# Performance work log

Measured on AMD Instinct MI355X. Metric: run time of the kernel, lower is better.

## Reference

```python
import jax, jax.numpy as jnp
import numpy as np

B, C, H, W = 4, 512, 96, 96
NH = 8
HD = C // NH
NC = 128
D = 768
L = H * W
EPS = 1e-5  # torch LayerNorm default


def _l2n(x, axis):
    # F.normalize: x / max(||x||, 1e-12)
    return x / jnp.maximum(jnp.linalg.norm(x, axis=axis, keepdims=True), 1e-12)


def _ln2d(x, g, b):
    # LayerNorm2d: normalize over channel dim of (B,C,H,W)
    mu = x.mean(1, keepdims=True)
    var = ((x - mu) ** 2).mean(1, keepdims=True)
    return (x - mu) / jnp.sqrt(var + EPS) * g[None, :, None, None] + b[None, :, None, None]


def _conv1x1(x, w):
    return jnp.einsum('oc,bchw->bohw', w, x)


def setup_inputs() -> dict:
    key = jax.random.key(0)
    ks = jax.random.split(key, 9)
    s = 0.02
    return {
        'img_feats': jax.random.normal(ks[0], (B, C, H, W), jnp.float32),
        'cls_embs': jax.random.normal(ks[1], (NC, D), jnp.float32),
        'cls_logits': jax.random.normal(ks[2], (B, NC), jnp.float32),
        'seg_logits': jax.random.normal(ks[3], (B, 1, H, W), jnp.float32),
        'gamma_g': jnp.ones((D,), jnp.float32), 'beta_g': jnp.zeros((D,), jnp.float32),
        'gamma_f': jnp.ones((C,), jnp.float32), 'beta_f': jnp.zeros((C,), jnp.float32),
        'attn_scale': jnp.ones((NH, 1, 1), jnp.float32),
        'Wg': jax.random.normal(ks[4], (C, D), jnp.float32) * s,
        'Wqkv': jax.random.normal(ks[5], (3 * C, C), jnp.float32) * s,
        'Wo': jax.random.normal(ks[6], (C, C), jnp.float32) * s,
        'bo': jnp.zeros((C,), jnp.float32),
        'gamma_n': jnp.ones((C,), jnp.float32), 'beta_n': jnp.zeros((C,), jnp.float32),
        'W1': jax.random.normal(ks[7], (C, C), jnp.float32) * s, 'b1': jnp.zeros((C,), jnp.float32),
        'W2': jax.random.normal(ks[8], (C, C), jnp.float32) * s, 'b2': jnp.zeros((C,), jnp.float32),
    }


def reference(img_feats, cls_embs, cls_logits, seg_logits, gamma_g, beta_g,
              gamma_f, beta_f, attn_scale, Wg, Wqkv, Wo, bo, gamma_n, beta_n,
              W1, b1, W2, b2):
    xn = _ln2d(img_feats, gamma_f, beta_f)
    # guide LayerNorm over embedding dim
    mu = cls_embs.mean(-1, keepdims=True)
    var = ((cls_embs - mu) ** 2).mean(-1, keepdims=True)
    cn = (cls_embs - mu) / jnp.sqrt(var + EPS) * gamma_g + beta_g
    g = (cn @ Wg.T).reshape(NC, NH, HD)  # nc nh hd

    qkv = _conv1x1(xn, Wqkv).reshape(B, 3, NH, HD, L)
    q, k, v = qkv[:, 0], qkv[:, 1], qkv[:, 2]  # each (B,NH,HD,L)

    # cosine guide map + min-max normalization + softmax-weighted aggregation over classes
    gm = jnp.einsum('nhd,bhdl->bhnl', _l2n(g, -1), _l2n(q, -2))
    gm = gm - gm.min(-1, keepdims=True)
    gm = gm / gm.max(-1, keepdims=True)
    gm = (jax.nn.softmax(gm, axis=2) * gm).sum(2, keepdims=True)  # (B,NH,1,L)

    # auxiliary guide map from cls logits + masked pooling of k
    cls_obj = jnp.einsum('nhd,bn->bhd', g, cls_logits)
    mask = jax.nn.sigmoid(seg_logits)  # (B,1,H,W)
    seg_obj = (mask * k.reshape(B, C, H, W)).sum((2, 3)) / mask.sum((2, 3))  # (B,C)
    obj = _l2n(cls_obj + seg_obj.reshape(B, NH, HD), -1)
    aux = jnp.einsum('bhd,bhdl->bhl', obj, _l2n(k, -2))[:, :, None, :]
    aux = aux - aux.min(-1, keepdims=True)
    aux = aux / aux.max(-1, keepdims=True)
    gm = gm * aux

    v = gm * v
    # channel (transposed) cosine attention: (B,NH,HD,HD)
    attn = jnp.einsum('bhdl,bhel->bhde', _l2n(q, -1), _l2n(k, -1)) * attn_scale
    out = jnp.einsum('bhde,bhel->bhdl', jax.nn.softmax(attn, -1), v).reshape(B, C, H, W)

    x = img_feats + _conv1x1(out, Wo) + bo[None, :, None, None]
    # ConvMlp with pre-norm: LayerNorm2d -> 1x1 conv -> GELU -> 1x1 conv
    fin = _ln2d(x, gamma_n, beta_n)
    h = jax.nn.gelu(_conv1x1(fin, W1) + b1[None, :, None, None], approximate=False)
    return x + _conv1x1(h, W2) + b2[None, :, None, None]
```

## Files before the change

kernel.cpp:

```cpp
#include <hip/hip_runtime.h>
#include <hip/hip_bf16.h>
#include <math.h>

#define BB 4
#define CC 512
#define NHEAD 8
#define HDIM 64
#define NCLS 128
#define DD 768
#define LL 9216
#define BLPIX 36864
#define EPSV 1e-5f
#define GMBLK 144
#define AUXBLK 144
#define LSPLIT 8
#define NLT 72
#define TP 132

typedef __hip_bfloat16 bf16;
typedef __attribute__((ext_vector_type(8))) short short8v;
typedef __attribute__((ext_vector_type(4))) short short4v;
typedef __attribute__((ext_vector_type(4))) float f32x4;

__device__ __forceinline__ float bf2f(bf16 v){ return __bfloat162float(v); }
__device__ __forceinline__ bf16 f2bf(float v){ return __float2bfloat16(v); }
__device__ __forceinline__ short bfbits(float v){ bf16 b = __float2bfloat16(v); return *reinterpret_cast<short*>(&b); }
__device__ __forceinline__ float s2f(short s){ bf16 b = *reinterpret_cast<bf16*>(&s); return __bfloat162float(b); }

__global__ __launch_bounds__(256) void wclsg_k(
    const float* __restrict__ wqkv, const float* __restrict__ wo,
    const float* __restrict__ w1, const float* __restrict__ w2,
    bf16* __restrict__ oq, bf16* __restrict__ oo,
    bf16* __restrict__ o1, bf16* __restrict__ o2,
    const float* __restrict__ cls_embs, const float* __restrict__ gamma_g,
    const float* __restrict__ beta_g, const float* __restrict__ Wg,
    float* __restrict__ g, bf16* __restrict__ gnb)
{
  __shared__ __align__(16) float cn[DD];
  __shared__ float red[256];
  __shared__ float gsh[CC];
  __shared__ float nrm[NHEAD];
  int bid = blockIdx.x;
  int tid = threadIdx.x;
  if (bid < 1536){
    int i = bid * 256 + tid;
    int e = i * 4;
    const float* src; bf16* dst; int off;
    if (e < 786432){ src = wqkv; dst = oq; off = e; }
    else if (e < 1048576){ src = wo; dst = oo; off = e - 786432; }
    else if (e < 1310720){ src = w1; dst = o1; off = e - 1048576; }
    else { src = w2; dst = o2; off = e - 1310720; }
    float4 v = *reinterpret_cast<const float4*>(src + off);
    short4v pk;
    pk[0] = bfbits(v.x); pk[1] = bfbits(v.y); pk[2] = bfbits(v.z); pk[3] = bfbits(v.w);
    *(short4v*)&dst[off] = pk;
    return;
  }
  {
    int n = bid - 1536;
    const float* e = cls_embs + (size_t)n * DD;
    float s = 0.f, ss = 0.f;
    for (int i = tid; i < DD; i += 256){ float v = e[i]; s += v; ss += v * v; }
    red[tid] = s; __syncthreads();
    for (int st = 128; st > 0; st >>= 1){ if (tid < st) red[tid] += red[tid + st]; __syncthreads(); }
    float mean = red[0] / DD; __syncthreads();
    red[tid] = ss; __syncthreads();
    for (int st = 128; st > 0; st >>= 1){ if (tid < st) red[tid] += red[tid + st]; __syncthreads(); }
    float var = red[0] / DD - mean * mean;
    float rstd = rsqrtf(var + EPSV);
    __syncthreads();
    for (int i = tid; i < DD; i += 256) cn[i] = (e[i] - mean) * rstd * gamma_g[i] + beta_g[i];
    __syncthreads();
    for (int c = tid; c < CC; c += 256){
      const float* w = Wg + (size_t)c * DD;
      float a = 0.f;
      #pragma unroll 8
      for (int d = 0; d < DD; d++) a += cn[d] * w[d];
      gsh[c] = a;
    }
    __syncthreads();
    if (tid < NHEAD){
      float a = 0.f;
      for (int d = 0; d < HDIM; d++){ float v = gsh[tid * HDIM + d]; a += v * v; }
      nrm[tid] = fmaxf(sqrtf(a), 1e-12f);
    }
    __syncthreads();
    for (int c = tid; c < CC; c += 256){
      g[(size_t)n * CC + c] = gsh[c];
      gnb[(size_t)n * CC + c] = f2bf(gsh[c] / nrm[c >> 6]);
    }
  }
}

__global__ __launch_bounds__(256, 2) void fuse_ln_k(const float* __restrict__ X,
    const float* __restrict__ lng, const float* __restrict__ lnb,
    bf16* __restrict__ xnT){
  __shared__ bf16 st[512][68];
  __shared__ float sred[2][4][64];
  __shared__ float muS[64], rsS[64];
  int p0 = blockIdx.x * 64;
  int b = p0 / LL, l0 = p0 - b * LL;
  int tid = threadIdx.x;
  #pragma unroll 4
  for (int i = 0; i < 32; i++){
    int idx = i * 256 + tid;
    int c = idx >> 4, l4 = (idx & 15) * 4;
    float4 v = *reinterpret_cast<const float4*>(X + (size_t)b * CC * LL + (size_t)c * LL + l0 + l4);
    short4v pk;
    pk[0] = bfbits(v.x); pk[1] = bfbits(v.y); pk[2] = bfbits(v.z); pk[3] = bfbits(v.w);
    *(short4v*)&st[c][l4] = pk;
  }
  __syncthreads();
  {
    int cg = tid >> 6, l = tid & 63;
    float s = 0.f, ss = 0.f;
    for (int c = cg * 128; c < cg * 128 + 128; c++){
      float v = bf2f(st[c][l]);
      s += v; ss += v * v;
    }
    sred[0][cg][l] = s; sred[1][cg][l] = ss;
  }
  __syncthreads();
  if (tid < 64){
    float st2 = sred[0][0][tid] + sred[0][1][tid] + sred[0][2][tid] + sred[0][3][tid];
    float sst = sred[1][0][tid] + sred[1][1][tid] + sred[1][2][tid] + sred[1][3][tid];
    float m = st2 * (1.0f / CC);
    float var = sst * (1.0f / CC) - m * m;
    muS[tid] = m; rsS[tid] = rsqrtf(var + EPSV);
  }
  __syncthreads();
  int pr = tid >> 4;
  int cc = (tid & 15) * 4;
  for (int cb = 0; cb < 8; cb++){
    int c0 = cb * 64;
    #pragma unroll
    for (int i = 0; i < 4; i++){
      int pl = pr + i * 16;
      int p = p0 + pl;
      float m = muS[pl], r = rsS[pl];
      short4v pk;
      #pragma unroll
      for (int e = 0; e < 4; e++){
        int c = c0 + cc + e;
        pk[e] = bfbits((bf2f(st[c][pl]) - m) * r * lng[c] + lnb[c]);
      }
      *(short4v*)&xnT[(size_t)p * CC + c0 + cc] = pk;
    }
  }
}

template<int MODE>
__global__ __launch_bounds__(256, 2) void mgemm_k(
    const bf16* __restrict__ A,
    const bf16* __restrict__ B,
    const float* __restrict__ residf,
    const bf16* __restrict__ residb,
    const float* __restrict__ bias,
    const float* __restrict__ lng, const float* __restrict__ lnb,
    float2* __restrict__ statp,
    float* __restrict__ qssp, float* __restrict__ kssp,
    bf16* __restrict__ qTo, float* __restrict__ rqo,
    bf16* __restrict__ ko, bf16* __restrict__ vo,
    bf16* __restrict__ xT_out,
    float* __restrict__ xo,
    bf16* __restrict__ ho,
    const float* __restrict__ gA, const float* __restrict__ clsl, float* __restrict__ clsovO,
    const float* __restrict__ segf, float* __restrict__ segpO)
{
  __shared__ __align__(16) short smem[128 * TP];
  __shared__ float sredf[512];
  short* Asm = smem;
  short* Bsm = smem + 8192;
  short* T   = smem;
  int tid = threadIdx.x;
  if (MODE == 0 && blockIdx.x >= 3456){
    int idx = (blockIdx.x - 3456) * 256 + tid;
    int b = idx >> 9, c = idx & 511;
    float a = 0.f;
    for (int n = 0; n < NCLS; n++) a += gA[(size_t)n * CC + c] * clsl[b * NCLS + n];
    clsovO[idx] = a;
    return;
  }
  int lane = tid & 63, wv = tid >> 6;
  int wr = wv >> 1, wc = wv & 1;
  int r15 = lane & 15, g = lane >> 4, h7 = lane & 7;
  int flat, gx, cpx;
  if (MODE == 0){ flat = blockIdx.x; gx = 12; cpx = 432; }
  else { gx = gridDim.x; flat = blockIdx.y * gx + blockIdx.x; cpx = (gx * gridDim.y) >> 3; }
  int swz = (flat & 7) * cpx + (flat >> 3);
  int m0 = (swz % gx) * 128, n0 = (swz / gx) * 128;
  int srow = tid >> 3, skkg = tid & 7;
  int sslot = ((skkg ^ (srow & 7))) * 8;

  f32x4 acc[4][4];
  #pragma unroll
  for (int i = 0; i < 4; i++)
    #pragma unroll
    for (int j = 0; j < 4; j++) acc[i][j] = (f32x4){0.f, 0.f, 0.f, 0.f};

  if (MODE == 2){
    if (tid < 128){
      int p = n0 + tid;
      float s = 0.f, ss2 = 0.f;
      #pragma unroll
      for (int part = 0; part < 4; part++){
        float2 v = statp[part * BLPIX + p];
        s += v.x; ss2 += v.y;
      }
      float m = s * (1.0f / CC);
      float var = ss2 * (1.0f / CC) - m * m;
      sredf[tid] = m;
      sredf[128 + tid] = rsqrtf(var + EPSV);
    }
    __syncthreads();
  }

  short8v pa[4], pb[4];
  auto loadAB = [&](int it){
    int k0 = it * 64;
    if (MODE == 2){
      int c0 = k0 + skkg * 8;
      float ga[8], be[8];
      *(float4*)&ga[0] = *(const float4*)&lng[c0];
      *(float4*)&ga[4] = *(const float4*)&lng[c0 + 4];
      *(float4*)&be[0] = *(const float4*)&lnb[c0];
      *(float4*)&be[4] = *(const float4*)&lnb[c0 + 4];
      #pragma unroll
      for (int r = 0; r < 4; r++){
        pa[r] = *reinterpret_cast<const short8v*>(A + (size_t)(m0 + r * 32 + srow) * 512 + c0);
        int rl = r * 32 + srow;
        float mm = sredf[rl], rr = sredf[128 + rl];
        short8v rawv = *reinterpret_cast<const short8v*>(B + (size_t)(n0 + rl) * 512 + c0);
        short8v ov;
        #pragma unroll
        for (int e = 0; e < 8; e++){
          float v = (s2f(rawv[e]) - mm) * rr * ga[e] + be[e];
          ov[e] = bfbits(v);
        }
        pb[r] = ov;
      }
    } else {
      #pragma unroll
      for (int r = 0; r < 4; r++){
        pa[r] = *reinterpret_cast<const short8v*>(A + (size_t)(m0 + r * 32 + srow) * 512 + k0 + skkg * 8);
        pb[r] = *reinterpret_cast<const short8v*>(B + (size_t)(n0 + r * 32 + srow) * 512 + k0 + skkg * 8);
      }
    }
  };

  loadAB(0);
  for (int it = 0; it < 8; ++it){
    __syncthreads();
    #pragma unroll
    for (int r = 0; r < 4; r++){
      int row = r * 32 + srow;
      *(short8v*)&Asm[row * 64 + sslot] = pa[r];
      *(short8v*)&Bsm[row * 64 + sslot] = pb[r];
    }
    __syncthreads();
    if (it < 7) loadAB(it + 1);
    #pragma unroll
    for (int s = 0; s < 2; s++){
      int slot = ((s * 4 + g) ^ h7) * 8;
      short8v af[4], bf_[4];
      #pragma unroll
      for (int i = 0; i < 4; i++){
        af[i]  = *(const short8v*)&Asm[(wr * 64 + i * 16 + r15) * 64 + slot];
        bf_[i] = *(const short8v*)&Bsm[(wc * 64 + i * 16 + r15) * 64 + slot];
      }
      #pragma unroll
      for (int i = 0; i < 4; i++)
        #pragma unroll
        for (int j = 0; j < 4; j++){
          if (MODE == 2)
            acc[i][j] = __builtin_amdgcn_mfma_f32_16x16x32_bf16(bf_[i], af[j], acc[i][j], 0, 0, 0);
          else
            acc[i][j] = __builtin_amdgcn_mfma_f32_16x16x32_bf16(af[i], bf_[j], acc[i][j], 0, 0, 0);
        }
    }
  }

  int bIdx = n0 / LL;
  int lbase = n0 - bIdx * LL;
  if (MODE == 0){
    int part = m0 >> 9;
    if (part == 0){
      int chb = m0 + wr * 64;
      int head = chb >> 6;
      int bh = bIdx * 8 + head;
      #pragma unroll
      for (int j = 0; j < 4; j++){
        float ssl = 0.f;
        #pragma unroll
        for (int i = 0; i < 4; i++)
          #pragma unroll
          for (int e = 0; e < 4; e++) ssl += acc[i][j][e] * acc[i][j][e];
        ssl += __shfl_xor(ssl, 16); ssl += __shfl_xor(ssl, 32);
        if (g == 0){
          int l = lbase + wc * 64 + j * 16 + r15;
          rqo[(size_t)bh * LL + l] = 1.0f / fmaxf(sqrtf(ssl), 1e-12f);
        }
      }
      #pragma unroll
      for (int i = 0; i < 4; i++)
        #pragma unroll
        for (int e = 0; e < 4; e++){
          float ssv = acc[i][0][e]*acc[i][0][e] + acc[i][1][e]*acc[i][1][e]
                    + acc[i][2][e]*acc[i][2][e] + acc[i][3][e]*acc[i][3][e];
          #pragma unroll
          for (int msk = 1; msk < 16; msk <<= 1) ssv += __shfl_xor(ssv, msk);
          if (r15 == 0) sredf[wv * 64 + i * 16 + g * 4 + e] = ssv;
        }
      __syncthreads();
      if (tid < 128){
        int wrr = tid >> 6, chL = tid & 63;
        float tot = sredf[(wrr * 2) * 64 + chL] + sredf[(wrr * 2 + 1) * 64 + chL];
        int c = m0 + wrr * 64 + chL;
        int row = bIdx * 512 + c;
        int ltile = lbase >> 7;
        qssp[(size_t)row * NLT + ltile] = tot;
      }
      #pragma unroll
      for (int i = 0; i < 4; i++)
        #pragma unroll
        for (int j = 0; j < 4; j++){
          int pxl = wc * 64 + j * 16 + r15;
          int chl = wr * 64 + i * 16 + g * 4;
          short4v pk;
          #pragma unroll
          for (int e = 0; e < 4; e++) pk[e] = bfbits(acc[i][j][e]);
          *(short4v*)&T[pxl * TP + chl] = pk;
        }
      __syncthreads();
      #pragma unroll
      for (int it2 = 0; it2 < 16; it2++){
        int c2 = tid + it2 * 256;
        int px = c2 >> 5, ch4 = (c2 & 31) * 4;
        *(short4v*)&qTo[((size_t)bIdx * LL + lbase + px) * CC + m0 + ch4] = *(short4v*)&T[px * TP + ch4];
      }
    } else if (part == 1){
      int chb = (m0 & 511) + wr * 64;
      #pragma unroll
      for (int i = 0; i < 4; i++)
        #pragma unroll
        for (int j = 0; j < 4; j++){
          int l = lbase + wc * 64 + j * 16 + r15;
          #pragma unroll
          for (int e = 0; e < 4; e++){
            int ch = chb + i * 16 + g * 4 + e;
            ko[(size_t)bIdx * CC * LL + (size_t)ch * LL + l] = f2bf(acc[i][j][e]);
          }
        }
      float sg[4];
      #pragma unroll
      for (int j = 0; j < 4; j++){
        int l = lbase + wc * 64 + j * 16 + r15;
        sg[j] = 1.0f / (1.0f + expf(-segf[(size_t)bIdx * LL + l]));
      }
      #pragma unroll
      for (int i = 0; i < 4; i++)
        #pragma unroll
        for (int e = 0; e < 4; e++){
          float ssv = acc[i][0][e]*acc[i][0][e] + acc[i][1][e]*acc[i][1][e]
                    + acc[i][2][e]*acc[i][2][e] + acc[i][3][e]*acc[i][3][e];
          float sgv = sg[0]*acc[i][0][e] + sg[1]*acc[i][1][e]
                    + sg[2]*acc[i][2][e] + sg[3]*acc[i][3][e];
          #pragma unroll
          for (int msk = 1; msk < 16; msk <<= 1){
            ssv += __shfl_xor(ssv, msk);
            sgv += __shfl_xor(sgv, msk);
          }
          if (r15 == 0){
            sredf[wv * 64 + i * 16 + g * 4 + e] = ssv;
            sredf[256 + wv * 64 + i * 16 + g * 4 + e] = sgv;
          }
        }
      __syncthreads();
      if (tid < 128){
        int wrr = tid >> 6, chL = tid & 63;
        float tot  = sredf[(wrr * 2) * 64 + chL] + sredf[(wrr * 2 + 1) * 64 + chL];
        float tots = sredf[256 + (wrr * 2) * 64 + chL] + sredf[256 + (wrr * 2 + 1) * 64 + chL];
        int c = (m0 & 511) + wrr * 64 + chL;
        int row = bIdx * 512 + c;
        int ltile = lbase >> 7;
        kssp[(size_t)row * NLT + ltile] = tot;
        segpO[(size_t)row * NLT + ltile] = tots;
      }
    } else {
      __syncthreads();
      #pragma unroll
      for (int i = 0; i < 4; i++)
        #pragma unroll
        for (int j = 0; j < 4; j++){
          int pxl = wc * 64 + j * 16 + r15;
          int chl = wr * 64 + i * 16 + g * 4;
          short4v pk;
          #pragma unroll
          for (int e = 0; e < 4; e++) pk[e] = bfbits(acc[i][j][e]);
          *(short4v*)&T[pxl * TP + chl] = pk;
        }
      __syncthreads();
      int chg = (m0 & 511);
      #pragma unroll
      for (int it2 = 0; it2 < 16; it2++){
        int c2 = tid + it2 * 256;
        int px = c2 >> 5, ch4 = (c2 & 31) * 4;
        *(short4v*)&vo[((size_t)bIdx * LL + lbase + px) * CC + chg + ch4] = *(short4v*)&T[px * TP + ch4];
      }
    }
  } else if (MODE == 1){
    __syncthreads();
    float sj[4] = {0.f,0.f,0.f,0.f}, ssj[4] = {0.f,0.f,0.f,0.f};
    #pragma unroll
    for (int i = 0; i < 4; i++)
      #pragma unroll
      for (int j = 0; j < 4; j++){
        int l = lbase + wc * 64 + j * 16 + r15;
        int chm = m0 + wr * 64 + i * 16 + g * 4;
        int pxl = wc * 64 + j * 16 + r15;
        int chl = wr * 64 + i * 16 + g * 4;
        short4v pk;
        #pragma unroll
        for (int e = 0; e < 4; e++){
          int m = chm + e;
          size_t o = (size_t)bIdx * CC * LL + (size_t)m * LL + l;
          float xv = residf[o] + acc[i][j][e] + bias[m];
          pk[e] = bfbits(xv);
          sj[j] += xv; ssj[j] += xv * xv;
        }
        *(short4v*)&T[pxl * TP + chl] = pk;
      }
    #pragma unroll
    for (int j = 0; j < 4; j++){
      sj[j] += __shfl_xor(sj[j], 16); sj[j] += __shfl_xor(sj[j], 32);
      ssj[j] += __shfl_xor(ssj[j], 16); ssj[j] += __shfl_xor(ssj[j], 32);
    }
    if (g == 0){
      #pragma unroll
      for (int j = 0; j < 4; j++){
        sredf[wv * 128 + j * 32 + r15 * 2 + 0] = sj[j];
        sredf[wv * 128 + j * 32 + r15 * 2 + 1] = ssj[j];
      }
    }
    __syncthreads();
    if (tid < 128){
      int wv2 = tid >> 6, lane2 = tid & 63, j2 = lane2 >> 4, r2 = lane2 & 15;
      float s   = sredf[wv2 * 128 + j2 * 32 + r2 * 2 + 0] + sredf[(wv2 + 2) * 128 + j2 * 32 + r2 * 2 + 0];
      float ss2 = sredf[wv2 * 128 + j2 * 32 + r2 * 2 + 1] + sredf[(wv2 + 2) * 128 + j2 * 32 + r2 * 2 + 1];
      int p = n0 + wv2 * 64 + j2 * 16 + r2;
      statp[(m0 >> 7) * BLPIX + p] = make_float2(s, ss2);
    }
    #pragma unroll
    for (int it2 = 0; it2 < 16; it2++){
      int c2 = tid + it2 * 256;
      int px = c2 >> 5, ch4 = (c2 & 31) * 4;
      *(short4v*)&xT_out[((size_t)bIdx * LL + lbase + px) * CC + m0 + ch4] = *(short4v*)&T[px * TP + ch4];
    }
  } else if (MODE == 3){
    __syncthreads();
    #pragma unroll
    for (int it2 = 0; it2 < 16; it2++){
      int c2 = tid + it2 * 256;
      int px = c2 >> 5, ch4 = (c2 & 31) * 4;
      *(short4v*)&T[px * TP + ch4] = *(const short4v*)&residb[((size_t)bIdx * LL + lbase + px) * CC + m0 + ch4];
    }
    __syncthreads();
    #pragma unroll
    for (int i = 0; i < 4; i++)
      #pragma unroll
      for (int j = 0; j < 4; j++){
        int l = lbase + wc * 64 + j * 16 + r15;
        int chm = m0 + wr * 64 + i * 16 + g * 4;
        int pxl = wc * 64 + j * 16 + r15;
        int chl = wr * 64 + i * 16 + g * 4;
        short4v rv = *(short4v*)&T[pxl * TP + chl];
        #pragma unroll
        for (int e = 0; e < 4; e++){
          int m = chm + e;
          size_t o = (size_t)bIdx * CC * LL + (size_t)m * LL + l;
          xo[o] = s2f(rv[e]) + acc[i][j][e] + bias[m];
        }
      }
  } else {
    #pragma unroll
    for (int i = 0; i < 4; i++)
      #pragma unroll
      for (int j = 0; j < 4; j++){
        int mm = m0 + wr * 64 + j * 16 + r15;
        float bv = bias[mm];
        #pragma unroll
        for (int e = 0; e < 4; e++){
          int n = n0 + wc * 64 + i * 16 + g * 4 + e;
          float t = acc[i][j][e] + bv;
          float gv = 0.5f * t * (1.0f + erff(t * 0.70710678118654752f));
          ho[(size_t)n * CC + mm] = f2bf(gv);
        }
      }
  }
}

__global__ __launch_bounds__(256) void mega1_k(
    const bf16* __restrict__ qT, const float* __restrict__ rq,
    const bf16* __restrict__ k, const bf16* __restrict__ gnb,
    float* __restrict__ pmin, float* __restrict__ pmax,
    float* __restrict__ part,
    const float* __restrict__ seg, float* __restrict__ seg_num, float* __restrict__ den,
    const float* __restrict__ qssp, const float* __restrict__ kssp,
    const float* __restrict__ segp,
    float* __restrict__ qn, float* __restrict__ kn)
{
  __shared__ __align__(16) bf16 qs[128 * 68];
  int bid = blockIdx.x;
  int t = threadIdx.x;
  if (bid < 1152){
    int bh = bid & 31, ltg = bid >> 5;
    int b = bh >> 3, h = bh & 7;
    int w = t >> 6, lane = t & 63, r15 = lane & 15, g = lane >> 4;
    short8v ag[2][2];
    #pragma unroll
    for (int i = 0; i < 2; i++)
      #pragma unroll
      for (int kt = 0; kt < 2; kt++)
        ag[i][kt] = *reinterpret_cast<const short8v*>(gnb + (size_t)(w * 32 + i * 16 + r15) * CC + h * 64 + kt * 32 + g * 8);
    for (int sub = 0; sub < 4; sub++){
      int lt = ltg * 4 + sub;
      int l0 = lt * 64;
      const bf16* qTp = qT + ((size_t)(b * LL + l0)) * CC + h * 64;
      short8v bq[4][2];
      float rqv[4];
      #pragma unroll
      for (int j = 0; j < 4; j++){
        #pragma unroll
        for (int kt = 0; kt < 2; kt++)
          bq[j][kt] = *reinterpret_cast<const short8v*>(qTp + (size_t)(j * 16 + r15) * CC + kt * 32 + g * 8);
        rqv[j] = rq[(size_t)bh * LL + l0 + j * 16 + r15];
      }
      f32x4 acc[2][4];
      #pragma unroll
      for (int i = 0; i < 2; i++)
        #pragma unroll
        for (int j = 0; j < 4; j++) acc[i][j] = (f32x4){0.f,0.f,0.f,0.f};
      #pragma unroll
      for (int kt = 0; kt < 2; kt++)
        #pragma unroll
        for (int i = 0; i < 2; i++)
          #pragma unroll
          for (int j = 0; j < 4; j++)
            acc[i][j] = __builtin_amdgcn_mfma_f32_16x16x32_bf16(ag[i][kt], bq[j][kt], acc[i][j], 0, 0, 0);
      #pragma unroll
      for (int i = 0; i < 2; i++)
        #pragma unroll
        for (int e = 0; e < 4; e++){
          float mn = 1e30f, mx = -1e30f;
          #pragma unroll
          for (int j = 0; j < 4; j++){
            float v = acc[i][j][e] * rqv[j];
            mn = fminf(mn, v); mx = fmaxf(mx, v);
          }
          #pragma unroll
          for (int msk = 1; msk < 16; msk <<= 1){
            mn = fminf(mn, __shfl_xor(mn, msk));
            mx = fmaxf(mx, __shfl_xor(mx, msk));
          }
          if (r15 == 0){
            int n = w * 32 + i * 16 + g * 4 + e;
            pmin[((size_t)bh * 128 + n) * GMBLK + lt] = mn;
            pmax[((size_t)bh * 128 + n) * GMBLK + lt] = mx;
          }
        }
    }
    return;
  }
  if (bid < 1408){
    int bid2 = bid - 1152;
    int ls = bid2 & 7, bh = bid2 >> 3;
    int b = bh >> 3, h = bh & 7;
    int w = t >> 6, lane = t & 63, r15 = lane & 15, g = lane >> 4;
    const bf16* kp = k + (size_t)b * CC * LL + (size_t)h * HDIM * LL;
    f32x4 acc4[4];
    #pragma unroll
    for (int j = 0; j < 4; j++) acc4[j] = (f32x4){0.f,0.f,0.f,0.f};
    for (int stg = 0; stg < 9; stg++){
      int lb = ls * 1152 + stg * 128;
      #pragma unroll
      for (int it = 0; it < 8; it++){
        int idx = t + it * 256;
        int row = idx >> 4, c4 = (idx & 15) * 4;
        *(short4v*)&qs[row * 68 + c4] = *(const short4v*)&qT[((size_t)(b * LL + lb + row)) * CC + h * 64 + c4];
      }
      __syncthreads();
      #pragma unroll
      for (int kstep = 0; kstep < 4; kstep++){
        int lloc = kstep * 32 + g * 8;
        short8v aq;
        #pragma unroll
        for (int jj = 0; jj < 8; jj++)
          aq[jj] = *reinterpret_cast<short*>(&qs[(lloc + jj) * 68 + w * 16 + r15]);
        int koff = lb + kstep * 32 + g * 8;
        short8v bk[4];
        #pragma unroll
        for (int j = 0; j < 4; j++) bk[j] = *reinterpret_cast<const short8v*>(kp + (size_t)(j * 16 + r15) * LL + koff);
        #pragma unroll
        for (int j = 0; j < 4; j++)
          acc4[j] = __builtin_amdgcn_mfma_f32_16x16x32_bf16(aq, bk[j], acc4[j], 0, 0, 0);
      }
      __syncthreads();
    }
    #pragma unroll
    for (int j = 0; j < 4; j++)
      #pragma unroll
      for (int e = 0; e < 4; e++){
        int d = w * 16 + g * 4 + e;
        int ee = j * 16 + r15;
        part[((size_t)(bh * LSPLIT + ls)) * 4096 + d * 64 + ee] = acc4[j][e];
      }
    return;
  }
  if (bid < 1412){
    float* red = (float*)qs;
    int b = bid - 1408;
    const float* sp = seg + (size_t)b * LL;
    float s = 0.f;
    for (int i = t; i < LL; i += 256) s += 1.0f / (1.0f + expf(-sp[i]));
    red[t] = s; __syncthreads();
    for (int st = 128; st > 0; st >>= 1){ if (t < st) red[t] += red[t + st]; __syncthreads(); }
    if (t == 0) den[b] = red[0];
    return;
  }
  {
    int r4 = (bid - 1412) * 4 + (t >> 6);
    int lane = t & 63;
    const float* src = (r4 < 2048) ? qssp : ((r4 < 4096) ? kssp : segp);
    int r = r4 & 2047;
    float s = src[(size_t)r * NLT + lane] + ((lane < 8) ? src[(size_t)r * NLT + 64 + lane] : 0.f);
    #pragma unroll
    for (int m = 1; m < 64; m <<= 1) s += __shfl_xor(s, m);
    if (lane == 0){
      if (r4 < 2048) qn[r] = fmaxf(sqrtf(s), 1e-12f);
      else if (r4 < 4096) kn[r] = fmaxf(sqrtf(s), 1e-12f);
      else seg_num[r] = s;
    }
  }
}

__global__ __launch_bounds__(256) void aux_k(const bf16* __restrict__ k,
                      const float* __restrict__ clsov, const float* __restrict__ segn,
                      const float* __restrict__ segd,
                      float* __restrict__ aux,
                      float* __restrict__ pmin, float* __restrict__ pmax){
  __shared__ bf16 ks[64 * 68];
  __shared__ float os[64];
  __shared__ float sspart[4][64], dotpart[4][64];
  int bh = blockIdx.x, lt = blockIdx.y;
  int l0 = lt * 64;
  int t = threadIdx.x;
  int b = bh >> 3, h = bh & 7;
  const bf16* kp = k + (size_t)b * CC * LL + (size_t)h * HDIM * LL + l0;
  #pragma unroll
  for (int i2 = 0; i2 < 4; i2++){
    int idx = t + i2 * 256;
    int d = idx >> 4, lch = (idx & 15) * 4;
    *(short4v*)&ks[d * 68 + lch] = *reinterpret_cast<const short4v*>(kp + (size_t)d * LL + lch);
  }
  if (t < 64){
    float sv = clsov[bh * 64 + t] + segn[bh * 64 + t] / segd[b];
    float ss2 = sv * sv;
    #pragma unroll
    for (int m = 1; m < 64; m <<= 1) ss2 += __shfl_xor(ss2, m);
    os[t] = sv / fmaxf(sqrtf(ss2), 1e-12f);
  }
  __syncthreads();
  {
    int dg = t >> 6, l = t & 63;
    float ssk = 0.f, dk = 0.f;
    #pragma unroll
    for (int dd = 0; dd < 16; dd++){
      float v = bf2f(ks[(dg * 16 + dd) * 68 + l]);
      ssk += v * v; dk += os[dg * 16 + dd] * v;
    }
    sspart[dg][l] = ssk; dotpart[dg][l] = dk;
  }
  __syncthreads();
  if (t < 64){
    float ss = sspart[0][t] + sspart[1][t] + sspart[2][t] + sspart[3][t];
    float dot = dotpart[0][t] + dotpart[1][t] + dotpart[2][t] + dotpart[3][t];
    float av = dot / fmaxf(sqrtf(ss), 1e-12f);
    aux[(size_t)bh * LL + l0 + t] = av;
    float mn = av, mx = av;
    #pragma unroll
    for (int m = 1; m < 64; m <<= 1){
      mn = fminf(mn, __shfl_xor(mn, m));
      mx = fmaxf(mx, __shfl_xor(mx, m));
    }
    if (t == 0){ pmin[bh * AUXBLK + lt] = mn; pmax[bh * AUXBLK + lt] = mx; }
  }
}

__global__ __launch_bounds__(256) void megared_k(
    const float* __restrict__ gpmin, const float* __restrict__ gpmax,
    float* __restrict__ gmin, float* __restrict__ gms,
    const float* __restrict__ apmin, const float* __restrict__ apmax,
    float* __restrict__ amin, float* __restrict__ ams,
    const float* __restrict__ part, const float* __restrict__ qn,
    const float* __restrict__ kn, const float* __restrict__ scale,
    bf16* __restrict__ Pb)
{
  __shared__ float As[64 * 65];
  int bid = blockIdx.x;
  int tid = threadIdx.x;
  if (bid < 1024){
    int row = bid * 4 + (tid >> 6);
    int lane = tid & 63;
    float mn = gpmin[(size_t)row * GMBLK + lane];
    float mx = gpmax[(size_t)row * GMBLK + lane];
    mn = fminf(mn, gpmin[(size_t)row * GMBLK + 64 + lane]);
    mx = fmaxf(mx, gpmax[(size_t)row * GMBLK + 64 + lane]);
    if (lane < 16){
      mn = fminf(mn, gpmin[(size_t)row * GMBLK + 128 + lane]);
      mx = fmaxf(mx, gpmax[(size_t)row * GMBLK + 128 + lane]);
    }
    #pragma unroll
    for (int m = 1; m < 64; m <<= 1){
      mn = fminf(mn, __shfl_xor(mn, m));
      mx = fmaxf(mx, __shfl_xor(mx, m));
    }
    if (lane == 0){ gmin[row] = mn; gms[row] = mx - mn; }
    return;
  }
  if (bid < 1032){
    int bh = (bid - 1024) * 4 + (tid >> 6);
    int lane = tid & 63;
    float mn = apmin[bh * AUXBLK + lane];
    float mx = apmax[bh * AUXBLK + lane];
    mn = fminf(mn, apmin[bh * AUXBLK + 64 + lane]);
    mx = fmaxf(mx, apmax[bh * AUXBLK + 64 + lane]);
    if (lane < 16){
      mn = fminf(mn, apmin[bh * AUXBLK + 128 + lane]);
      mx = fmaxf(mx, apmax[bh * AUXBLK + 128 + lane]);
    }
    #pragma unroll
    for (int m = 1; m < 64; m <<= 1){
      mn = fminf(mn, __shfl_xor(mn, m));
      mx = fmaxf(mx, __shfl_xor(mx, m));
    }
    if (lane == 0){ amin[bh] = mn; ams[bh] = mx - mn; }
    return;
  }
  {
    int bh = bid - 1032;
    int h = bh & 7;
    #pragma unroll
    for (int i = 0; i < 16; i++){
      int cell = tid + i * 256;
      int d = cell >> 6, e = cell & 63;
      float s = 0.f;
      #pragma unroll
      for (int ls = 0; ls < LSPLIT; ls++) s += part[((size_t)(bh * LSPLIT + ls)) * 4096 + cell];
      As[d * 65 + e] = s * scale[h] / (qn[bh * 64 + d] * kn[bh * 64 + e]);
    }
    __syncthreads();
    if (tid < 64){
      int d = tid;
      float mx = -1e30f;
      for (int e = 0; e < 64; e++) mx = fmaxf(mx, As[d * 65 + e]);
      float sum = 0.f;
      for (int e = 0; e < 64; e++){ float ev = expf(As[d * 65 + e] - mx); As[d * 65 + e] = ev; sum += ev; }
      float inv = 1.0f / sum;
      for (int e = 0; e < 64; e++) Pb[(size_t)bh * 4096 + d * 64 + e] = f2bf(As[d * 65 + e] * inv);
    }
  }
}

__global__ __launch_bounds__(256) void pv_k(const bf16* __restrict__ qT, const float* __restrict__ rq,
      const bf16* __restrict__ gnb,
      const float* __restrict__ aux,
      const float* __restrict__ gmin, const float* __restrict__ gms,
      const float* __restrict__ amin, const float* __restrict__ ams,
      const bf16* __restrict__ Pb, const bf16* __restrict__ vT, bf16* __restrict__ outT){
  __shared__ float gminS[128], rgmsS[128];
  __shared__ float separt[4][64], setpart[4][64];
  __shared__ float wl[64];
  int bh = blockIdx.x, lt = blockIdx.y;
  int l0 = lt * 64;
  int t = threadIdx.x;
  int b = bh >> 3, h = bh & 7;
  int w = t >> 6, lane = t & 63, r15 = lane & 15, g = lane >> 4;
  if (t < 128){ gminS[t] = gmin[bh * 128 + t]; rgmsS[t] = 1.0f / gms[bh * 128 + t]; }
  short8v ag[2][2];
  #pragma unroll
  for (int i = 0; i < 2; i++)
    #pragma unroll
    for (int kt = 0; kt < 2; kt++)
      ag[i][kt] = *reinterpret_cast<const short8v*>(gnb + (size_t)(w * 32 + i * 16 + r15) * CC + h * 64 + kt * 32 + g * 8);
  const bf16* qTp = qT + ((size_t)(b * LL + l0)) * CC + h * 64;
  short8v bq[4][2];
  float rqv[4];
  #pragma unroll
  for (int j = 0; j < 4; j++){
    #pragma unroll
    for (int kt = 0; kt < 2; kt++)
      bq[j][kt] = *reinterpret_cast<const short8v*>(qTp + (size_t)(j * 16 + r15) * CC + kt * 32 + g * 8);
    rqv[j] = rq[(size_t)bh * LL + l0 + j * 16 + r15];
  }
  f32x4 acc[2][4];
  #pragma unroll
  for (int i = 0; i < 2; i++)
    #pragma unroll
    for (int j = 0; j < 4; j++) acc[i][j] = (f32x4){0.f,0.f,0.f,0.f};
  #pragma unroll
  for (int kt = 0; kt < 2; kt++)
    #pragma unroll
    for (int i = 0; i < 2; i++)
      #pragma unroll
      for (int j = 0; j < 4; j++)
        acc[i][j] = __builtin_amdgcn_mfma_f32_16x16x32_bf16(ag[i][kt], bq[j][kt], acc[i][j], 0, 0, 0);
  __syncthreads();
  float seL[4] = {0.f,0.f,0.f,0.f}, setL[4] = {0.f,0.f,0.f,0.f};
  #pragma unroll
  for (int i = 0; i < 2; i++)
    #pragma unroll
    for (int j = 0; j < 4; j++)
      #pragma unroll
      for (int e = 0; e < 4; e++){
        int n = w * 32 + i * 16 + g * 4 + e;
        float tt = (acc[i][j][e] * rqv[j] - gminS[n]) * rgmsS[n];
        float ee = __expf(tt);
        seL[j] += ee; setL[j] += ee * tt;
      }
  #pragma unroll
  for (int j = 0; j < 4; j++){
    seL[j] += __shfl_xor(seL[j], 16); seL[j] += __shfl_xor(seL[j], 32);
    setL[j] += __shfl_xor(setL[j], 16); setL[j] += __shfl_xor(setL[j], 32);
  }
  if (g == 0){
    #pragma unroll
    for (int j = 0; j < 4; j++){ separt[w][j * 16 + r15] = seL[j]; setpart[w][j * 16 + r15] = setL[j]; }
  }
  __syncthreads();
  if (t < 64){
    float se = separt[0][t] + separt[1][t] + separt[2][t] + separt[3][t];
    float st = setpart[0][t] + setpart[1][t] + setpart[2][t] + setpart[3][t];
    float gmred = st / se;
    float auxn = (aux[(size_t)bh * LL + l0 + t] - amin[bh]) / ams[bh];
    wl[t] = gmred * auxn;
  }
  __syncthreads();
  short8v ap[4][2];
  #pragma unroll
  for (int i = 0; i < 4; i++)
    #pragma unroll
    for (int kt = 0; kt < 2; kt++)
      ap[i][kt] = *reinterpret_cast<const short8v*>(Pb + (size_t)bh * 4096 + (i * 16 + r15) * 64 + kt * 32 + g * 8);
  const bf16* vrow = vT + ((size_t)b * LL + l0 + w * 16 + r15) * CC + h * 64;
  short8v bv[2];
  #pragma unroll
  for (int kt = 0; kt < 2; kt++) bv[kt] = *reinterpret_cast<const short8v*>(vrow + kt * 32 + g * 8);
  f32x4 oacc[4];
  #pragma unroll
  for (int i = 0; i < 4; i++) oacc[i] = (f32x4){0.f,0.f,0.f,0.f};
  #pragma unroll
  for (int kt = 0; kt < 2; kt++)
    #pragma unroll
    for (int i = 0; i < 4; i++)
      oacc[i] = __builtin_amdgcn_mfma_f32_16x16x32_bf16(ap[i][kt], bv[kt], oacc[i], 0, 0, 0);
  float wlv = wl[w * 16 + r15];
  bf16* orow = outT + ((size_t)b * LL + l0 + w * 16 + r15) * CC + h * 64;
  #pragma unroll
  for (int i = 0; i < 4; i++){
    short4v pk;
    #pragma unroll
    for (int e = 0; e < 4; e++) pk[e] = bfbits(oacc[i][e] * wlv);
    *(short4v*)&orow[i * 16 + g * 4] = pk;
  }
}

extern "C" void kernel_launch(void* const* d_in, const int* in_sizes, int n_in,
                              void* d_out, int out_size, void* d_ws, size_t ws_size,
                              hipStream_t stream){
  const float* img        = (const float*)d_in[0];
  const float* cls_embs   = (const float*)d_in[1];
  const float* cls_logits = (const float*)d_in[2];
  const float* seg        = (const float*)d_in[3];
  const float* gamma_g    = (const float*)d_in[4];
  const float* beta_g     = (const float*)d_in[5];
  const float* gamma_f    = (const float*)d_in[6];
  const float* beta_f     = (const float*)d_in[7];
  const float* attn_scale = (const float*)d_in[8];
  const float* Wg         = (const float*)d_in[9];
  const float* Wqkv       = (const float*)d_in[10];
  const float* Wo         = (const float*)d_in[11];
  const float* bo         = (const float*)d_in[12];
  const float* gamma_n    = (const float*)d_in[13];
  const float* beta_n     = (const float*)d_in[14];
  const float* W1         = (const float*)d_in[15];
  const float* b1         = (const float*)d_in[16];
  const float* W2         = (const float*)d_in[17];
  const float* b2         = (const float*)d_in[18];
  float* outp = (float*)d_out;
  (void)in_sizes; (void)n_in; (void)out_size;

  char* wsb = (char*)d_ws;
  size_t off = 0;
  auto alloc = [&](size_t bytes)->char*{
    char* p = wsb + off;
    off += (bytes + 255) & ~(size_t)255;
    return p;
  };
  float2* statp= (float2*)alloc((size_t)4 * BLPIX * 8);
  float* qssp  = (float*)alloc((size_t)2048 * NLT * 4);
  float* kssp  = (float*)alloc((size_t)2048 * NLT * 4);
  float* segp  = (float*)alloc((size_t)2048 * NLT * 4);
  float* qn    = (float*)alloc(2048 * 4);
  float* kn    = (float*)alloc(2048 * 4);
  float* rqb   = (float*)alloc((size_t)32 * LL * 4);
  float* gbuf  = (float*)alloc((size_t)NCLS * CC * 4);
  bf16*  gnbb  = (bf16*)alloc((size_t)NCLS * CC * 2);
  float* clsov = (float*)alloc(2048 * 4);
  float* segn  = (float*)alloc(2048 * 4);
  float* segd  = (float*)alloc(256);
  float* gminp = (float*)alloc((size_t)32 * 128 * GMBLK * 4);
  float* gmaxp = (float*)alloc((size_t)32 * 128 * GMBLK * 4);
  float* gminv = (float*)alloc(4096 * 4);
  float* gmsv  = (float*)alloc(4096 * 4);
  float* auxv  = (float*)alloc((size_t)32 * LL * 4);
  float* apmin = (float*)alloc(32 * AUXBLK * 4);
  float* apmax = (float*)alloc(32 * AUXBLK * 4);
  float* aminv = (float*)alloc(256);
  float* amsv  = (float*)alloc(256);
  bf16*  Pb    = (bf16*)alloc((size_t)32 * 4096 * 2);
  float* apart = (float*)alloc((size_t)32 * LSPLIT * 4096 * 4);
  bf16* qb    = (bf16*)alloc((size_t)BB * CC * LL * 2);
  bf16* kb    = (bf16*)alloc((size_t)BB * CC * LL * 2);
  bf16* wqkvb = (bf16*)alloc((size_t)1536 * 512 * 2);
  bf16* wob   = (bf16*)alloc((size_t)512 * 512 * 2);
  bf16* w1b   = (bf16*)alloc((size_t)512 * 512 * 2);
  bf16* w2b   = (bf16*)alloc((size_t)512 * 512 * 2);
  bf16* vT  = (bf16*)d_out;
  bf16* xnT = (bf16*)((char*)d_out + (size_t)BB * CC * LL * 2);
  bf16* qTb = qb;
  bf16* outT = kb;
  bf16* xT   = qb;
  bf16* hbT  = kb;
  if (off > ws_size) return;

  wclsg_k<<<1664, 256, 0, stream>>>(Wqkv, Wo, W1, W2, wqkvb, wob, w1b, w2b,
      cls_embs, gamma_g, beta_g, Wg, gbuf, gnbb);
  fuse_ln_k<<<576, 256, 0, stream>>>(img, gamma_f, beta_f, xnT);
  mgemm_k<0><<<3464, 256, 0, stream>>>(wqkvb, xnT, nullptr, nullptr, nullptr,
      nullptr, nullptr, nullptr, qssp, kssp,
      qTb, rqb, kb, vT, nullptr, nullptr, nullptr,
      gbuf, cls_logits, clsov, seg, segp);
  mega1_k<<<2948, 256, 0, stream>>>(qTb, rqb, kb, gnbb, gminp, gmaxp, apart,
      seg, segn, segd, qssp, kssp, segp, qn, kn);
  aux_k<<<dim3(32, 144), 256, 0, stream>>>(kb, clsov, segn, segd, auxv, apmin, apmax);
  megared_k<<<1064, 256, 0, stream>>>(gminp, gmaxp, gminv, gmsv,
      apmin, apmax, aminv, amsv,
      apart, qn, kn, attn_scale, Pb);
  pv_k<<<dim3(32, GMBLK), 256, 0, stream>>>(qTb, rqb, gnbb, auxv, gminv, gmsv, aminv, amsv, Pb, vT, outT);
  mgemm_k<1><<<dim3(4, 288), 256, 0, stream>>>(wob, outT, img, nullptr, bo,
      nullptr, nullptr, statp, nullptr, nullptr,
      nullptr, nullptr, nullptr, nullptr, xT, nullptr, nullptr,
      nullptr, nullptr, nullptr, nullptr, nullptr);
  mgemm_k<2><<<dim3(4, 288), 256, 0, stream>>>(w1b, xT, nullptr, nullptr, b1,
      gamma_n, beta_n, statp, nullptr, nullptr,
      nullptr, nullptr, nullptr, nullptr, nullptr, nullptr, hbT,
      nullptr, nullptr, nullptr, nullptr, nullptr);
  mgemm_k<3><<<dim3(4, 288), 256, 0, stream>>>(w2b, hbT, nullptr, xT, b2,
      nullptr, nullptr, nullptr, nullptr, nullptr,
      nullptr, nullptr, nullptr, nullptr, nullptr, outp, nullptr,
      nullptr, nullptr, nullptr, nullptr, nullptr);
}
```

Baseline: 440.0 us.

## Fuse guide-map q·g min/max partials into the QKV GEMM epilogue

The guide-map GEMM (normalized guide embeddings times q) and its per-tile min/max partials move out of mega1_k into the q-part epilogue of the QKV GEMM. The epilogue reuses the q tile already staged in shared memory, plus per-pixel inverse norms stashed in shared memory. This removes a re-read of qT and rq from global memory and 1152 blocks from mega1_k. In exchange the q-producing GEMM blocks carry extra MFMA work, guide-matrix loads and register pressure, which could lengthen that kernel's tail.

After: 448.0 us. No clear change (+1.8%).

```diff
diff --git a/kernel.cpp b/kernel.cpp
--- a/kernel.cpp
+++ b/kernel.cpp
@@ -165,7 +165,8 @@
     float* __restrict__ xo,
     bf16* __restrict__ ho,
     const float* __restrict__ gA, const float* __restrict__ clsl, float* __restrict__ clsovO,
-    const float* __restrict__ segf, float* __restrict__ segpO)
+    const float* __restrict__ segf, float* __restrict__ segpO,
+    const bf16* __restrict__ gnbA, float* __restrict__ pminO, float* __restrict__ pmaxO)
 {
   __shared__ __align__(16) short smem[128 * TP];
   __shared__ float sredf[512];
@@ -296,9 +297,11 @@
           #pragma unroll
           for (int e = 0; e < 4; e++) ssl += acc[i][j][e] * acc[i][j][e];
         ssl += __shfl_xor(ssl, 16); ssl += __shfl_xor(ssl, 32);
+        float rqv_ = 1.0f / fmaxf(sqrtf(ssl), 1e-12f);
         if (g == 0){
           int l = lbase + wc * 64 + j * 16 + r15;
-          rqo[(size_t)bh * LL + l] = 1.0f / fmaxf(sqrtf(ssl), 1e-12f);
+          rqo[(size_t)bh * LL + l] = rqv_;
+          sredf[256 + wr * 128 + wc * 64 + j * 16 + r15] = rqv_;
         }
       }
       #pragma unroll
@@ -337,6 +340,65 @@
         int c2 = tid + it2 * 256;
         int px = c2 >> 5, ch4 = (c2 & 31) * 4;
         *(short4v*)&qTo[((size_t)bIdx * LL + lbase + px) * CC + m0 + ch4] = *(short4v*)&T[px * TP + ch4];
+      }
+      {
+        int h0 = m0 >> 6;
+        int ltb = lbase >> 6;
+        #pragma unroll
+        for (int hh = 0; hh < 2; hh++){
+          int bh2 = bIdx * 8 + h0 + hh;
+          short8v ag2[2][2];
+          #pragma unroll
+          for (int i = 0; i < 2; i++)
+            #pragma unroll
+            for (int kt = 0; kt < 2; kt++)
+              ag2[i][kt] = *reinterpret_cast<const short8v*>(gnbA + (size_t)(wv * 32 + i * 16 + r15) * CC + (h0 + hh) * 64 + kt * 32 + g * 8);
+          #pragma unroll
+          for (int ph = 0; ph < 2; ph++){
+            short8v bq2[4][2];
+            float rqv2[4];
+            #pragma unroll
+            for (int j = 0; j < 4; j++){
+              #pragma unroll
+              for (int kt = 0; kt < 2; kt++)
+                bq2[j][kt] = *reinterpret_cast<const short8v*>(&T[(ph * 64 + j * 16 + r15) * TP + hh * 64 + kt * 32 + g * 8]);
+              rqv2[j] = sredf[256 + hh * 128 + ph * 64 + j * 16 + r15];
+            }
+            f32x4 acc2[2][4];
+            #pragma unroll
+            for (int i = 0; i < 2; i++)
+              #pragma unroll
+              for (int j = 0; j < 4; j++) acc2[i][j] = (f32x4){0.f,0.f,0.f,0.f};
+            #pragma unroll
+            for (int kt = 0; kt < 2; kt++)
+              #pragma unroll
+              for (int i = 0; i < 2; i++)
+                #pragma unroll
+                for (int j = 0; j < 4; j++)
+                  acc2[i][j] = __builtin_amdgcn_mfma_f32_16x16x32_bf16(ag2[i][kt], bq2[j][kt], acc2[i][j], 0, 0, 0);
+            #pragma unroll
+            for (int i = 0; i < 2; i++)
+              #pragma unroll
+              for (int e = 0; e < 4; e++){
+                float mn = 1e30f, mx = -1e30f;
+                #pragma unroll
+                for (int j = 0; j < 4; j++){
+                  float v = acc2[i][j][e] * rqv2[j];
+                  mn = fminf(mn, v); mx = fmaxf(mx, v);
+                }
+                #pragma unroll
+                for (int msk = 1; msk < 16; msk <<= 1){
+                  mn = fminf(mn, __shfl_xor(mn, msk));
+                  mx = fmaxf(mx, __shfl_xor(mx, msk));
+                }
+                if (r15 == 0){
+                  int n = wv * 32 + i * 16 + g * 4 + e;
+                  pminO[((size_t)bh2 * 128 + n) * GMBLK + ltb + ph] = mn;
+                  pmaxO[((size_t)bh2 * 128 + n) * GMBLK + ltb + ph] = mx;
+                }
+              }
+          }
+        }
       }
     } else if (part == 1){
       int chb = (m0 & 511) + wr * 64;
@@ -512,68 +574,9 @@
   __shared__ __align__(16) bf16 qs[128 * 68];
   int bid = blockIdx.x;
   int t = threadIdx.x;
-  if (bid < 1152){
-    int bh = bid & 31, ltg = bid >> 5;
-    int b = bh >> 3, h = bh & 7;
-    int w = t >> 6, lane = t & 63, r15 = lane & 15, g = lane >> 4;
-    short8v ag[2][2];
-    #pragma unroll
-    for (int i = 0; i < 2; i++)
-      #pragma unroll
-      for (int kt = 0; kt < 2; kt++)
-        ag[i][kt] = *reinterpret_cast<const short8v*>(gnb + (size_t)(w * 32 + i * 16 + r15) * CC + h * 64 + kt * 32 + g * 8);
-    for (int sub = 0; sub < 4; sub++){
-      int lt = ltg * 4 + sub;
-      int l0 = lt * 64;
-      const bf16* qTp = qT + ((size_t)(b * LL + l0)) * CC + h * 64;
-      short8v bq[4][2];
-      float rqv[4];
-      #pragma unroll
-      for (int j = 0; j < 4; j++){
-        #pragma unroll
-        for (int kt = 0; kt < 2; kt++)
-          bq[j][kt] = *reinterpret_cast<const short8v*>(qTp + (size_t)(j * 16 + r15) * CC + kt * 32 + g * 8);
-        rqv[j] = rq[(size_t)bh * LL + l0 + j * 16 + r15];
-      }
-      f32x4 acc[2][4];
-      #pragma unroll
-      for (int i = 0; i < 2; i++)
-        #pragma unroll
-        for (int j = 0; j < 4; j++) acc[i][j] = (f32x4){0.f,0.f,0.f,0.f};
-      #pragma unroll
-      for (int kt = 0; kt < 2; kt++)
-        #pragma unroll
-        for (int i = 0; i < 2; i++)
-          #pragma unroll
-          for (int j = 0; j < 4; j++)
-            acc[i][j] = __builtin_amdgcn_mfma_f32_16x16x32_bf16(ag[i][kt], bq[j][kt], acc[i][j], 0, 0, 0);
-      #pragma unroll
-      for (int i = 0; i < 2; i++)
-        #pragma unroll
-        for (int e = 0; e < 4; e++){
-          float mn = 1e30f, mx = -1e30f;
-          #pragma unroll
-          for (int j = 0; j < 4; j++){
-            float v = acc[i][j][e] * rqv[j];
-            mn = fminf(mn, v); mx = fmaxf(mx, v);
-          }
-          #pragma unroll
-          for (int msk = 1; msk < 16; msk <<= 1){
-            mn = fminf(mn, __shfl_xor(mn, msk));
-            mx = fmaxf(mx, __shfl_xor(mx, msk));
-          }
-          if (r15 == 0){
-            int n = w * 32 + i * 16 + g * 4 + e;
-            pmin[((size_t)bh * 128 + n) * GMBLK + lt] = mn;
-            pmax[((size_t)bh * 128 + n) * GMBLK + lt] = mx;
-          }
-        }
-    }
-    return;
-  }
-  if (bid < 1408){
-    int bid2 = bid - 1152;
-    int ls = bid2 & 7, bh = bid2 >> 3;
+  (void)rq; (void)gnb; (void)pmin; (void)pmax;
+  if (bid < 256){
+    int ls = bid & 7, bh = bid >> 3;
     int b = bh >> 3, h = bh & 7;
     int w = t >> 6, lane = t & 63, r15 = lane & 15, g = lane >> 4;
     const bf16* kp = k + (size_t)b * CC * LL + (size_t)h * HDIM * LL;
@@ -616,9 +619,9 @@
       }
     return;
   }
-  if (bid < 1412){
+  if (bid < 260){
     float* red = (float*)qs;
-    int b = bid - 1408;
+    int b = bid - 256;
     const float* sp = seg + (size_t)b * LL;
     float s = 0.f;
     for (int i = t; i < LL; i += 256) s += 1.0f / (1.0f + expf(-sp[i]));
@@ -628,7 +631,7 @@
     return;
   }
   {
-    int r4 = (bid - 1412) * 4 + (t >> 6);
+    int r4 = (bid - 260) * 4 + (t >> 6);
     int lane = t & 63;
     const float* src = (r4 < 2048) ? qssp : ((r4 < 4096) ? kssp : segp);
     int r = r4 & 2047;
@@ -949,8 +952,9 @@
   mgemm_k<0><<<3464, 256, 0, stream>>>(wqkvb, xnT, nullptr, nullptr, nullptr,
       nullptr, nullptr, nullptr, qssp, kssp,
       qTb, rqb, kb, vT, nullptr, nullptr, nullptr,
-      gbuf, cls_logits, clsov, seg, segp);
-  mega1_k<<<2948, 256, 0, stream>>>(qTb, rqb, kb, gnbb, gminp, gmaxp, apart,
+      gbuf, cls_logits, clsov, seg, segp,
+      gnbb, gminp, gmaxp);
+  mega1_k<<<1796, 256, 0, stream>>>(qTb, rqb, kb, gnbb, gminp, gmaxp, apart,
       seg, segn, segd, qssp, kssp, segp, qn, kn);
   aux_k<<<dim3(32, 144), 256, 0, stream>>>(kb, clsov, segn, segd, auxv, apmin, apmax);
   megared_k<<<1064, 256, 0, stream>>>(gminp, gmaxp, gminv, gmsv,
@@ -960,13 +964,16 @@
   mgemm_k<1><<<dim3(4, 288), 256, 0, stream>>>(wob, outT, img, nullptr, bo,
       nullptr, nullptr, statp, nullptr, nullptr,
       nullptr, nullptr, nullptr, nullptr, xT, nullptr, nullptr,
-      nullptr, nullptr, nullptr, nullptr, nullptr);
+      nullptr, nullptr, nullptr, nullptr, nullptr,
+      nullptr, nullptr, nullptr);
   mgemm_k<2><<<dim3(4, 288), 256, 0, stream>>>(w1b, xT, nullptr, nullptr, b1,
       gamma_n, beta_n, statp, nullptr, nullptr,
       nullptr, nullptr, nullptr, nullptr, nullptr, nullptr, hbT,
-      nullptr, nullptr, nullptr, nullptr, nullptr);
+      nullptr, nullptr, nullptr, nullptr, nullptr,
+      nullptr, nullptr, nullptr);
   mgemm_k<3><<<dim3(4, 288), 256, 0, stream>>>(w2b, hbT, nullptr, xT, b2,
       nullptr, nullptr, nullptr, nullptr, nullptr,
       nullptr, nullptr, nullptr, nullptr, nullptr, outp, nullptr,
-      nullptr, nullptr, nullptr, nullptr, nullptr);
+      nullptr, nullptr, nullptr, nullptr, nullptr,
+      nullptr, nullptr, nullptr);
 }
```
